# Optimization experiments

Hardware: AMD Instinct MI355X
Metric: run time of the kernel (lower is better)

The kernel has to match this reference:

```python
import jax, jax.numpy as jnp
import numpy as np

CAUSAL = True

def setup_inputs() -> dict:
    key = jax.random.key(0)
    kq, kk, kv = jax.random.split(key, 3)
    B, S, H, D = 2, 2048, 16, 64
    q = jax.random.normal(kq, (B, S, H, D), dtype=jnp.float32)
    k = jax.random.normal(kk, (B, S, H, D), dtype=jnp.float32)
    v = jax.random.normal(kv, (B, S, H, D), dtype=jnp.float32)
    return {"q": q, "k": k, "v": v}

def reference(q, k, v):
    # q,k,v: [B, S, H, D]
    B, Sq, H, D = q.shape
    Sk = k.shape[1]
    scale = 1.0 / jnp.sqrt(jnp.asarray(D, dtype=q.dtype))
    # scores: [B, H, Sq, Sk]
    scores = jnp.einsum('bqhd,bkhd->bhqk', q * scale, k)
    if CAUSAL:
        causal_mask = jnp.triu(jnp.ones((Sq, Sk), dtype=bool), k=1)
        scores = jnp.where(causal_mask, -jnp.inf, scores)
    attn = jax.nn.softmax(scores, axis=-1)
    # output: [B, Sq, H, D]
    out = jnp.einsum('bhqk,bkhd->bqhd', attn, v)
    return out
```

## Files before the change

kernel.cpp:

```cpp
#include <hip/hip_runtime.h>


typedef __bf16  bf16x8_t  __attribute__((ext_vector_type(8)));
typedef short   short8_t  __attribute__((ext_vector_type(8)));
typedef float   f32x4     __attribute__((ext_vector_type(4)));

#define MFMA_K32(a, b, c) __builtin_amdgcn_mfma_f32_16x16x32_bf16((a), (b), (c), 0, 0, 0)
#define BC8(x) __builtin_bit_cast(bf16x8_t, (x))

constexpr int   SEQ = 2048, NH = 16;
constexpr int   SROW = NH * 64;
constexpr float QS   = 0.125f * 1.44269504088896f;

__device__ __forceinline__ unsigned f2bfu(float f) {
    unsigned u = __builtin_bit_cast(unsigned, f);
    return (u + 0x7fffu + ((u >> 16) & 1u)) >> 16;
}
__device__ __forceinline__ unsigned pk2(float x, float y) {
#if defined(__HIP_DEVICE_COMPILE__) && __has_builtin(__builtin_amdgcn_cvt_pk_bf16_f32)
    typedef __bf16 bfv2 __attribute__((ext_vector_type(2)));
    bfv2 v = __builtin_amdgcn_cvt_pk_bf16_f32(x, y);
    return __builtin_bit_cast(unsigned, v);
#else
    return (f2bfu(x) & 0xffffu) | (f2bfu(y) << 16);
#endif
}

__global__ __launch_bounds__(256) void prepack(const float* __restrict__ K,
                                               const float* __restrict__ V,
                                               unsigned short* __restrict__ Kp,
                                               unsigned short* __restrict__ Vp) {
    const int blk = blockIdx.x;
    const int tid = threadIdx.x;
    if (blk < 1024) {
        const int bh = blk >> 5, c = blk & 31;
        const int b  = bh >> 4,  h = bh & 15;
        const int nt = tid >> 6, lane = tid & 63;
        const int llo = lane & 15, lhi = lane >> 4;
        const float* src = K + (size_t)(b * SEQ + c * 64 + nt * 16 + llo) * SROW + h * 64;
#pragma unroll
        for (int ks = 0; ks < 2; ++ks) {
            const float4* p = (const float4*)(src + ks * 32 + lhi * 8);
            float4 a = p[0], d4 = p[1];
            uint4 u;
            u.x = pk2(a.x, a.y);   u.y = pk2(a.z, a.w);
            u.z = pk2(d4.x, d4.y); u.w = pk2(d4.z, d4.w);
            *(uint4*)(Kp + (size_t)(bh * 32 + c) * 4096 + (nt * 2 + ks) * 512 + lane * 8) = u;
        }
    } else {
        const int q  = blk - 1024;
        const int bh = q >> 5, c = q & 31;
        const int b  = bh >> 4, h = bh & 15;
        const int dt = tid >> 6, lane = tid & 63;
        const int llo = lane & 15, lhi = lane >> 4;
#pragma unroll
        for (int g2 = 0; g2 < 2; ++g2) {
            const int g = c * 2 + g2;
            const float* base = V + (size_t)(b * SEQ + g * 32 + 4 * lhi) * SROW + h * 64 + dt * 16 + llo;
            float f0 = base[0],            f1 = base[SROW],
                  f2 = base[2 * SROW],     f3 = base[3 * SROW];
            const float* b2 = base + 16 * SROW;
            float f4 = b2[0],              f5 = b2[SROW],
                  f6 = b2[2 * SROW],       f7 = b2[3 * SROW];
            uint4 u;
            u.x = pk2(f0, f1); u.y = pk2(f2, f3);
            u.z = pk2(f4, f5); u.w = pk2(f6, f7);
            *(uint4*)(Vp + (size_t)(bh * 64 + g) * 2048 + dt * 512 + lane * 8) = u;
        }
    }
}

__global__ __launch_bounds__(256, 4) void fa_fwd(const float* __restrict__ Q,
                                                 const unsigned short* __restrict__ Kp,
                                                 const unsigned short* __restrict__ Vp,
                                                 float* __restrict__ O) {
    const int id = blockIdx.x;
    const int bh = id & 31;
    const int T  = 63 - (id >> 5);
    const int b  = bh >> 4, h = bh & 15;
    const int NSC = (T + 4) >> 2;
    const int q0  = T * 32;

    const int tid  = threadIdx.x;
    const int w    = tid >> 6;
    const int lane = tid & 63;
    const int lhi  = lane >> 4;
    const int llo  = lane & 15;

    __shared__ __align__(16) float Red[4][5][64][4];

    const char* Ku = (const char*)Kp + ((size_t)bh << 18);
    const char* Vu = (const char*)Vp + ((size_t)bh << 18);
    int kov = (w << 12) + lane * 16;
    int vov = (w << 12) + lane * 16;

    bf16x8_t qf[2][2];
#pragma unroll
    for (int mt = 0; mt < 2; ++mt)
#pragma unroll
        for (int ks = 0; ks < 2; ++ks) {
            const float* qp = Q + (size_t)(b * SEQ + q0 + mt * 16 + llo) * SROW + h * 64 + ks * 32 + lhi * 8;
            float4 a = ((const float4*)qp)[0], c4 = ((const float4*)qp)[1];
            uint4 u;
            u.x = pk2(a.x * QS, a.y * QS); u.y = pk2(a.z * QS, a.w * QS);
            u.z = pk2(c4.x * QS, c4.y * QS); u.w = pk2(c4.z * QS, c4.w * QS);
            qf[mt][ks] = __builtin_bit_cast(bf16x8_t, u);
        }

    f32x4 acc[2][4], accL[2];
#pragma unroll
    for (int mt = 0; mt < 2; ++mt) {
        accL[mt] = (f32x4){0.f, 0.f, 0.f, 0.f};
#pragma unroll
        for (int dt = 0; dt < 4; ++dt) acc[mt][dt] = (f32x4){0.f, 0.f, 0.f, 0.f};
    }

    short8_t o8;
#pragma unroll
    for (int j = 0; j < 8; ++j) o8[j] = (short)0x3F80;
    const bf16x8_t ones8 = __builtin_bit_cast(bf16x8_t, o8);

    uint4 kc[4];
#pragma unroll
    for (int i = 0; i < 4; ++i) kc[i] = *(const uint4*)(Ku + kov + i * 1024);

    for (int sc = 0; sc < NSC; ++sc) {
        uint4 vc[4];
#pragma unroll
        for (int dt = 0; dt < 4; ++dt) vc[dt] = *(const uint4*)(Vu + vov + dt * 1024);

        const int kb = (sc << 7) + (w << 5);
        const int m_g0 = q0 + llo;

        {
            f32x4 s0 = (f32x4){0.f, 0.f, 0.f, 0.f};
            f32x4 s1 = (f32x4){0.f, 0.f, 0.f, 0.f};
            s0 = MFMA_K32(BC8(kc[0]), qf[0][0], s0);
            s0 = MFMA_K32(BC8(kc[1]), qf[0][1], s0);
            s1 = MFMA_K32(BC8(kc[2]), qf[0][0], s1);
            s1 = MFMA_K32(BC8(kc[3]), qf[0][1], s1);

            if (kb + 15 > q0) {
#pragma unroll
                for (int r = 0; r < 4; ++r)
                    if (kb + lhi * 4 + r > m_g0) s0[r] = -INFINITY;
            }
            if (kb + 31 > q0) {
#pragma unroll
                for (int r = 0; r < 4; ++r)
                    if (kb + 16 + lhi * 4 + r > m_g0) s1[r] = -INFINITY;
            }

            uint4 up;
            up.x = pk2(__builtin_amdgcn_exp2f(s0[0]), __builtin_amdgcn_exp2f(s0[1]));
            up.y = pk2(__builtin_amdgcn_exp2f(s0[2]), __builtin_amdgcn_exp2f(s0[3]));
            up.z = pk2(__builtin_amdgcn_exp2f(s1[0]), __builtin_amdgcn_exp2f(s1[1]));
            up.w = pk2(__builtin_amdgcn_exp2f(s1[2]), __builtin_amdgcn_exp2f(s1[3]));
            const bf16x8_t pf = BC8(up);

#pragma unroll
            for (int dt = 0; dt < 4; ++dt)
                acc[0][dt] = MFMA_K32(pf, BC8(vc[dt]), acc[0][dt]);
            accL[0] = MFMA_K32(pf, ones8, accL[0]);
        }

        {
            f32x4 s0 = (f32x4){0.f, 0.f, 0.f, 0.f};
            f32x4 s1 = (f32x4){0.f, 0.f, 0.f, 0.f};
            s0 = MFMA_K32(BC8(kc[0]), qf[1][0], s0);
            s0 = MFMA_K32(BC8(kc[1]), qf[1][1], s0);
            s1 = MFMA_K32(BC8(kc[2]), qf[1][0], s1);
            s1 = MFMA_K32(BC8(kc[3]), qf[1][1], s1);

            kov += 16384;
#pragma unroll
            for (int i = 0; i < 4; ++i) kc[i] = *(const uint4*)(Ku + kov + i * 1024);

            const int m0  = q0 + 16;
            const int m_g = m0 + llo;
            if (kb + 15 > m0) {
#pragma unroll
                for (int r = 0; r < 4; ++r)
                    if (kb + lhi * 4 + r > m_g) s0[r] = -INFINITY;
            }
            if (kb + 31 > m0) {
#pragma unroll
                for (int r = 0; r < 4; ++r)
                    if (kb + 16 + lhi * 4 + r > m_g) s1[r] = -INFINITY;
            }

            uint4 up;
            up.x = pk2(__builtin_amdgcn_exp2f(s0[0]), __builtin_amdgcn_exp2f(s0[1]));
            up.y = pk2(__builtin_amdgcn_exp2f(s0[2]), __builtin_amdgcn_exp2f(s0[3]));
            up.z = pk2(__builtin_amdgcn_exp2f(s1[0]), __builtin_amdgcn_exp2f(s1[1]));
            up.w = pk2(__builtin_amdgcn_exp2f(s1[2]), __builtin_amdgcn_exp2f(s1[3]));
            const bf16x8_t pf = BC8(up);

#pragma unroll
            for (int dt = 0; dt < 4; ++dt)
                acc[1][dt] = MFMA_K32(pf, BC8(vc[dt]), acc[1][dt]);
            accL[1] = MFMA_K32(pf, ones8, accL[1]);
        }

        vov += 16384;
    }

#pragma unroll
    for (int mt = 0; mt < 2; ++mt) {
#pragma unroll
        for (int dt = 0; dt < 4; ++dt) *(f32x4*)&Red[w][dt][lane][0] = acc[mt][dt];
        *(f32x4*)&Red[w][4][lane][0] = accL[mt];
        __syncthreads();
        f32x4 oc = (f32x4){0.f, 0.f, 0.f, 0.f};
        f32x4 ls = (f32x4){0.f, 0.f, 0.f, 0.f};
#pragma unroll
        for (int u = 0; u < 4; ++u) {
            oc += *(const f32x4*)&Red[u][w][lane][0];
            ls += *(const f32x4*)&Red[u][4][lane][0];
        }
#pragma unroll
        for (int r = 0; r < 4; ++r)
            O[(size_t)(b * SEQ + q0 + mt * 16 + lhi * 4 + r) * SROW + h * 64 + w * 16 + llo] = oc[r] / ls[r];
        __syncthreads();
    }
}

extern "C" void kernel_launch(void* const* d_in, const int* in_sizes, int n_in,
                              void* d_out, int out_size, void* d_ws, size_t ws_size,
                              hipStream_t stream) {
    const float* q = (const float*)d_in[0];
    const float* k = (const float*)d_in[1];
    const float* v = (const float*)d_in[2];
    float* o = (float*)d_out;
    unsigned short* Kp = (unsigned short*)d_ws;
    unsigned short* Vp = Kp + (size_t)32 * 32 * 4096;
    prepack<<<dim3(2048), dim3(256), 0, stream>>>(k, v, Kp, Vp);
    fa_fwd<<<dim3(2048), dim3(256), 0, stream>>>(q, Kp, Vp, o);
}
```

Measured before the change: 122.7 us.

## Double-buffer V tiles in LDS via direct global-to-LDS loads, add MFMA priority hints

V fragments are no longer loaded from global memory into registers each iteration. They are now prefetched one step ahead with global_load_lds into a per-wave double buffer in shared memory and read back from LDS just before the PV MFMAs. The kernel also wraps MFMA groups in s_setprio, interleaves the QK MFMAs, raises the launch-bounds occupancy hint from 4 to 5 blocks, and reuses the 32KB LDS buffer for the final reduction. The aim is to cut VGPR pressure and hide V load latency, at the cost of extra LDS traffic. It relies on the compiler inserting the right vmcnt waits before the LDS reads.

```diff
diff --git a/kernel.cpp b/kernel.cpp
--- a/kernel.cpp
+++ b/kernel.cpp
@@ -23,6 +23,14 @@
     return __builtin_bit_cast(unsigned, v);
 #else
     return (f2bfu(x) & 0xffffu) | (f2bfu(y) << 16);
+#endif
+}
+
+__device__ __forceinline__ void gload_lds16(const void* g, void* l) {
+#if defined(__HIP_DEVICE_COMPILE__)
+    __builtin_amdgcn_global_load_lds(
+        (const __attribute__((address_space(1))) unsigned*)g,
+        (__attribute__((address_space(3))) unsigned*)l, 16, 0, 0);
 #endif
 }
 
@@ -70,7 +78,7 @@
     }
 }
 
-__global__ __launch_bounds__(256, 4) void fa_fwd(const float* __restrict__ Q,
+__global__ __launch_bounds__(256, 5) void fa_fwd(const float* __restrict__ Q,
                                                  const unsigned short* __restrict__ Kp,
                                                  const unsigned short* __restrict__ Vp,
                                                  float* __restrict__ O) {
@@ -87,7 +95,8 @@
     const int lhi  = lane >> 4;
     const int llo  = lane & 15;
 
-    __shared__ __align__(16) float Red[4][5][64][4];
+    __shared__ __align__(16) unsigned char LB[32768];
+    unsigned char* VLw = LB + w * 8192;
 
     const char* Ku = (const char*)Kp + ((size_t)bh << 18);
     const char* Vu = (const char*)Vp + ((size_t)bh << 18);
@@ -120,26 +129,30 @@
     for (int j = 0; j < 8; ++j) o8[j] = (short)0x3F80;
     const bf16x8_t ones8 = __builtin_bit_cast(bf16x8_t, o8);
 
+#pragma unroll
+    for (int dt = 0; dt < 4; ++dt)
+        gload_lds16(Vu + vov + dt * 1024, VLw + dt * 1024);
+    vov += 16384;
     uint4 kc[4];
 #pragma unroll
     for (int i = 0; i < 4; ++i) kc[i] = *(const uint4*)(Ku + kov + i * 1024);
 
     for (int sc = 0; sc < NSC; ++sc) {
-        uint4 vc[4];
-#pragma unroll
-        for (int dt = 0; dt < 4; ++dt) vc[dt] = *(const uint4*)(Vu + vov + dt * 1024);
-
+        unsigned char* cur = VLw + ((sc & 1) << 12);
+        unsigned char* nxt = VLw + (((sc & 1) ^ 1) << 12);
         const int kb = (sc << 7) + (w << 5);
-        const int m_g0 = q0 + llo;
 
         {
+            __builtin_amdgcn_s_setprio(1);
             f32x4 s0 = (f32x4){0.f, 0.f, 0.f, 0.f};
             f32x4 s1 = (f32x4){0.f, 0.f, 0.f, 0.f};
             s0 = MFMA_K32(BC8(kc[0]), qf[0][0], s0);
+            s1 = MFMA_K32(BC8(kc[2]), qf[0][0], s1);
             s0 = MFMA_K32(BC8(kc[1]), qf[0][1], s0);
-            s1 = MFMA_K32(BC8(kc[2]), qf[0][0], s1);
             s1 = MFMA_K32(BC8(kc[3]), qf[0][1], s1);
-
+            __builtin_amdgcn_s_setprio(0);
+
+            const int m_g0 = q0 + llo;
             if (kb + 15 > q0) {
 #pragma unroll
                 for (int r = 0; r < 4; ++r)
@@ -158,32 +171,38 @@
             up.w = pk2(__builtin_amdgcn_exp2f(s1[2]), __builtin_amdgcn_exp2f(s1[3]));
             const bf16x8_t pf = BC8(up);
 
-#pragma unroll
-            for (int dt = 0; dt < 4; ++dt)
-                acc[0][dt] = MFMA_K32(pf, BC8(vc[dt]), acc[0][dt]);
+            __builtin_amdgcn_s_setprio(1);
+#pragma unroll
+            for (int dt = 0; dt < 4; ++dt) {
+                uint4 vf = *(const uint4*)(cur + dt * 1024 + lane * 16);
+                acc[0][dt] = MFMA_K32(pf, BC8(vf), acc[0][dt]);
+            }
             accL[0] = MFMA_K32(pf, ones8, accL[0]);
+            __builtin_amdgcn_s_setprio(0);
         }
 
         {
+            __builtin_amdgcn_s_setprio(1);
             f32x4 s0 = (f32x4){0.f, 0.f, 0.f, 0.f};
             f32x4 s1 = (f32x4){0.f, 0.f, 0.f, 0.f};
             s0 = MFMA_K32(BC8(kc[0]), qf[1][0], s0);
+            s1 = MFMA_K32(BC8(kc[2]), qf[1][0], s1);
             s0 = MFMA_K32(BC8(kc[1]), qf[1][1], s0);
-            s1 = MFMA_K32(BC8(kc[2]), qf[1][0], s1);
             s1 = MFMA_K32(BC8(kc[3]), qf[1][1], s1);
+            __builtin_amdgcn_s_setprio(0);
 
             kov += 16384;
 #pragma unroll
             for (int i = 0; i < 4; ++i) kc[i] = *(const uint4*)(Ku + kov + i * 1024);
 
-            const int m0  = q0 + 16;
-            const int m_g = m0 + llo;
-            if (kb + 15 > m0) {
+            const int m1  = q0 + 16;
+            const int m_g = m1 + llo;
+            if (kb + 15 > m1) {
 #pragma unroll
                 for (int r = 0; r < 4; ++r)
                     if (kb + lhi * 4 + r > m_g) s0[r] = -INFINITY;
             }
-            if (kb + 31 > m0) {
+            if (kb + 31 > m1) {
 #pragma unroll
                 for (int r = 0; r < 4; ++r)
                     if (kb + 16 + lhi * 4 + r > m_g) s1[r] = -INFINITY;
@@ -196,15 +215,25 @@
             up.w = pk2(__builtin_amdgcn_exp2f(s1[2]), __builtin_amdgcn_exp2f(s1[3]));
             const bf16x8_t pf = BC8(up);
 
-#pragma unroll
-            for (int dt = 0; dt < 4; ++dt)
-                acc[1][dt] = MFMA_K32(pf, BC8(vc[dt]), acc[1][dt]);
+            __builtin_amdgcn_s_setprio(1);
+#pragma unroll
+            for (int dt = 0; dt < 4; ++dt) {
+                uint4 vf = *(const uint4*)(cur + dt * 1024 + lane * 16);
+                acc[1][dt] = MFMA_K32(pf, BC8(vf), acc[1][dt]);
+            }
             accL[1] = MFMA_K32(pf, ones8, accL[1]);
-        }
-
+            __builtin_amdgcn_s_setprio(0);
+        }
+
+#pragma unroll
+        for (int dt = 0; dt < 4; ++dt)
+            gload_lds16(Vu + vov + dt * 1024, nxt + dt * 1024);
         vov += 16384;
     }
 
+    __syncthreads();
+    typedef float RedT[5][64][4];
+    RedT* Red = (RedT*)LB;
 #pragma unroll
     for (int mt = 0; mt < 2; ++mt) {
 #pragma unroll
```

New measurement: 174.4 us. 1.42x slower.
